# Kernel optimization log

Measured on AMD Instinct MI355X. Metric: run time of the kernel, lower is better.

Reference implementation:

```python
import jax, jax.numpy as jnp
import numpy as np

B, L, D, H, U = 1024, 256, 256, 512, 512


def setup_inputs() -> dict:
    key = jax.random.key(0)
    ks = jax.random.split(key, 5)
    scale_f = 1.0
    return {
        "features": jax.random.normal(ks[0], (B, L, D), dtype=jnp.float32),
        "hidden": jax.random.normal(ks[1], (B, H), dtype=jnp.float32),
        "W1": jax.random.normal(ks[2], (D, U), dtype=jnp.float32) / np.sqrt(D),
        "b1": jnp.zeros((U,), dtype=jnp.float32),
        "W2": jax.random.normal(ks[3], (H, U), dtype=jnp.float32) / np.sqrt(H),
        "b2": jnp.zeros((U,), dtype=jnp.float32),
        "Wv": jax.random.normal(ks[4], (U, 1), dtype=jnp.float32) / np.sqrt(U),
        "bv": jnp.zeros((1,), dtype=jnp.float32),
    }


def reference(features, hidden, W1, b1, W2, b2, Wv, bv):
    # features: [B, L, D], hidden: [B, H]
    proj_f = jnp.einsum("bld,du->blu", features, W1) + b1      # [B, L, U]
    proj_h = (hidden @ W2 + b2)[:, None, :]                      # [B, 1, U]
    score = jnp.tanh(proj_f + proj_h)                            # [B, L, U]
    logits = jnp.einsum("blu,uo->blo", score, Wv) + bv           # [B, L, 1]
    attention_weights = jax.nn.softmax(logits, axis=1)           # [B, L, 1]
    context_vector = jnp.sum(attention_weights * features, axis=1)  # [B, D]
    return (context_vector, attention_weights)
```

## Files before the change

### kernel.cpp

```cpp
#include <hip/hip_runtime.h>
#include <hip/hip_bf16.h>

#define B_ 1024
#define L_ 256
#define D_ 256
#define H_ 512
#define U_ 512
#define M_ (B_ * L_)

#define BM 128

typedef float f32x4 __attribute__((ext_vector_type(4)));
typedef short bf16x8 __attribute__((ext_vector_type(8)));
typedef short bf16x4 __attribute__((ext_vector_type(4)));

__device__ __forceinline__ short f2bf(float f) {
  unsigned u = __float_as_uint(f);
  u += 0x7fffu + ((u >> 16) & 1u);
  return (short)(u >> 16);
}

__device__ __forceinline__ float fast_tanh(float x) {
  float e = __expf(2.0f * x);
  return 1.0f - 2.0f * __builtin_amdgcn_rcpf(e + 1.0f);
}

__global__ void k_w1f(const float* __restrict__ W1, short* __restrict__ W1F) {
  int i = blockIdx.x * 256 + threadIdx.x;
  int jj = i & 7;
  int no = (i >> 3) & 15;
  int kc = (i >> 7) & 3;
  int kb = (i >> 9) & 7;
  int nb = i >> 12;
  int u = nb * 16 + no;
  int d = kb * 32 + kc * 8 + jj;
  W1F[i] = f2bf(W1[(size_t)d * U_ + u]);
}

__global__ void k_projh(const float* __restrict__ hidden, const float* __restrict__ W2,
                        const float* __restrict__ b1, const float* __restrict__ b2,
                        float* __restrict__ ph) {
  int u = blockIdx.x * 256 + threadIdx.x;
  int b0 = blockIdx.y * 8;
  float acc[8] = {0.f, 0.f, 0.f, 0.f, 0.f, 0.f, 0.f, 0.f};
  for (int h = 0; h < H_; ++h) {
    float w = W2[(size_t)h * U_ + u];
#pragma unroll
    for (int i = 0; i < 8; ++i) acc[i] = fmaf(hidden[(size_t)(b0 + i) * H_ + h], w, acc[i]);
  }
  float bias = b1[u] + b2[u];
#pragma unroll
  for (int i = 0; i < 8; ++i) ph[(size_t)(b0 + i) * U_ + u] = acc[i] + bias;
}

__global__ __launch_bounds__(256, 2) void k_gemm(
    const float* __restrict__ F,
    const short* __restrict__ W1F,
    const float* __restrict__ ph,
    const float* __restrict__ Wv,
    float* __restrict__ logits) {
  __shared__ __align__(16) short As[BM * D_];
  __shared__ float csum[2][BM];

  const int tid = threadIdx.x;
  const int lane = tid & 63;
  const int hi = lane >> 4;
  const int wid = tid >> 6;
  const int wr = wid >> 1, wc = wid & 1;
  const int m0 = blockIdx.x * BM;
  const int b = m0 >> 8;

  {
    const float* sp = F + (size_t)(m0 + (tid >> 6)) * D_ + (tid & 63) * 4;
    const int kq8 = (tid & 63) * 8;
#pragma unroll
    for (int jb = 0; jb < 2; ++jb) {
      f32x4 sv[16];
#pragma unroll
      for (int j = 0; j < 16; ++j)
        sv[j] = *(const f32x4*)(sp + (size_t)(jb * 16 + j) * 4 * D_);
#pragma unroll
      for (int j = 0; j < 16; ++j) {
        int row = (jb * 16 + j) * 4 + (tid >> 6);
        int boff = (row * 512 + kq8) ^ ((row & 7) << 4);
        bf16x4 w;
#pragma unroll
        for (int q = 0; q < 4; ++q) w[q] = f2bf(sv[j][q]);
        *(bf16x4*)((char*)As + boff) = w;
      }
    }
  }
  __syncthreads();

  f32x4 acc[4][4];
  float cs[4][4];
  const f32x4 fz = {0.f, 0.f, 0.f, 0.f};
#pragma unroll
  for (int mi = 0; mi < 4; ++mi)
#pragma unroll
    for (int x = 0; x < 4; ++x) { acc[mi][x] = fz; cs[mi][x] = 0.f; }

  const short* bbase = W1F + (size_t)(wc * 32) * 512 + lane * 8;
  bf16x8 bcur[4], bnxt[4];
#pragma unroll
  for (int ni = 0; ni < 4; ++ni)
    bcur[ni] = *(const bf16x8*)(bbase + (size_t)(ni * 8) * 512);

  const float* phr = ph + (size_t)b * U_;
  const int rbase = wr * 64 + (lane & 15);

  for (int nt = 0; nt < 4; ++nt) {
#pragma unroll
    for (int kt = 0; kt < 8; ++kt) {
      if (nt * 8 + kt < 31) {
        const int ktn = (kt + 1) & 7;
        const int ntn64 = (nt + ((kt + 1) >> 3)) * 64;
#pragma unroll
        for (int ni = 0; ni < 4; ++ni)
          bnxt[ni] = *(const bf16x8*)(bbase + (size_t)(ntn64 + ni * 8 + ktn) * 512);
      }
      bf16x8 af[4];
#pragma unroll
      for (int mi = 0; mi < 4; ++mi) {
        int rA = rbase + mi * 16;
        int boff = (rA * 512 + kt * 64 + hi * 16) ^ ((rA & 7) << 4);
        af[mi] = *(const bf16x8*)((const char*)As + boff);
      }
#pragma unroll
      for (int mi = 0; mi < 4; ++mi) {
        acc[mi][0] = __builtin_amdgcn_mfma_f32_16x16x32_bf16(af[mi], bcur[0], acc[mi][0], 0, 0, 0);
        acc[mi][1] = __builtin_amdgcn_mfma_f32_16x16x32_bf16(af[mi], bcur[1], acc[mi][1], 0, 0, 0);
        acc[mi][2] = __builtin_amdgcn_mfma_f32_16x16x32_bf16(af[mi], bcur[2], acc[mi][2], 0, 0, 0);
        acc[mi][3] = __builtin_amdgcn_mfma_f32_16x16x32_bf16(af[mi], bcur[3], acc[mi][3], 0, 0, 0);
      }
#pragma unroll
      for (int ni = 0; ni < 4; ++ni) bcur[ni] = bnxt[ni];
    }
#pragma unroll
    for (int ni = 0; ni < 4; ++ni) {
      int u = nt * 128 + wc * 64 + ni * 16 + (lane & 15);
      float phv = phr[u];
      float wvv = Wv[u];
#pragma unroll
      for (int mi = 0; mi < 4; ++mi) {
#pragma unroll
        for (int r = 0; r < 4; ++r) {
          float x = acc[mi][ni][r] + phv;
          cs[mi][r] += fast_tanh(x) * wvv;
        }
      }
    }
#pragma unroll
    for (int mi = 0; mi < 4; ++mi)
#pragma unroll
      for (int x = 0; x < 4; ++x) acc[mi][x] = fz;
  }

#pragma unroll
  for (int mi = 0; mi < 4; ++mi) {
#pragma unroll
    for (int off = 1; off < 16; off <<= 1) {
#pragma unroll
      for (int r = 0; r < 4; ++r) cs[mi][r] += __shfl_xor(cs[mi][r], off);
    }
    if ((lane & 15) == 0) {
      int rloc = wr * 64 + mi * 16 + hi * 4;
#pragma unroll
      for (int r = 0; r < 4; ++r) csum[wc][rloc + r] = cs[mi][r];
    }
  }
  __syncthreads();
  if (tid < BM) logits[m0 + tid] = csum[0][tid] + csum[1][tid];
}

__global__ void k_smctx(const float* __restrict__ logits, const float* __restrict__ F,
                        float* __restrict__ outw, float* __restrict__ ctx) {
  __shared__ float wl[L_];
  __shared__ f32x4 part[256];
  __shared__ float red[8];
  int b = blockIdx.x, t = threadIdx.x;
  float x = logits[(size_t)b * L_ + t];
  float m = x;
#pragma unroll
  for (int off = 32; off >= 1; off >>= 1) m = fmaxf(m, __shfl_xor(m, off));
  if ((t & 63) == 0) red[t >> 6] = m;
  __syncthreads();
  m = fmaxf(fmaxf(red[0], red[1]), fmaxf(red[2], red[3]));
  float e = __expf(x - m);
  float s = e;
#pragma unroll
  for (int off = 32; off >= 1; off >>= 1) s += __shfl_xor(s, off);
  if ((t & 63) == 0) red[4 + (t >> 6)] = s;
  __syncthreads();
  s = (red[4] + red[5]) + (red[6] + red[7]);
  float w = e / s;
  outw[(size_t)b * L_ + t] = w;
  wl[t] = w;
  __syncthreads();

  int lq = t >> 6, dq = t & 63;
  const f32x4* F4 = (const f32x4*)(F + (size_t)b * L_ * D_);
  f32x4 acc = {0.f, 0.f, 0.f, 0.f};
  for (int l = lq; l < L_; l += 4) acc += wl[l] * F4[l * 64 + dq];
  part[t] = acc;
  __syncthreads();
  if (lq == 0) {
    f32x4 r = (part[t] + part[t + 64]) + (part[t + 128] + part[t + 192]);
    ((f32x4*)ctx)[(size_t)b * 64 + dq] = r;
  }
}

extern "C" void kernel_launch(void* const* d_in, const int* in_sizes, int n_in,
                              void* d_out, int out_size, void* d_ws, size_t ws_size,
                              hipStream_t stream) {
  const float* F      = (const float*)d_in[0];
  const float* hidden = (const float*)d_in[1];
  const float* W1     = (const float*)d_in[2];
  const float* b1     = (const float*)d_in[3];
  const float* W2     = (const float*)d_in[4];
  const float* b2     = (const float*)d_in[5];
  const float* Wv     = (const float*)d_in[6];

  float* out_ctx = (float*)d_out;
  float* out_w   = out_ctx + (size_t)B_ * D_;

  char* ws = (char*)d_ws;
  short* W1F    = (short*)ws;
  float* ph     = (float*)(ws + 262144);
  float* logits = (float*)(ws + 262144 + 2097152);

  k_w1f<<<512, 256, 0, stream>>>(W1, W1F);
  k_projh<<<dim3(2, 128), 256, 0, stream>>>(hidden, W2, b1, b2, ph);
  k_gemm<<<2048, 256, 0, stream>>>(F, W1F, ph, Wv, logits);
  k_smctx<<<1024, 256, 0, stream>>>(logits, F, out_w, out_ctx);
}
```

Before: 254.8 us.

## Split GEMM over N tiles with direct global A loads and atomic logit accumulation

```diff
diff --git a/kernel.cpp b/kernel.cpp
--- a/kernel.cpp
+++ b/kernel.cpp
@@ -12,7 +12,6 @@
 
 typedef float f32x4 __attribute__((ext_vector_type(4)));
 typedef short bf16x8 __attribute__((ext_vector_type(8)));
-typedef short bf16x4 __attribute__((ext_vector_type(4)));
 
 __device__ __forceinline__ short f2bf(float f) {
   unsigned u = __float_as_uint(f);
@@ -53,13 +52,12 @@
   for (int i = 0; i < 8; ++i) ph[(size_t)(b0 + i) * U_ + u] = acc[i] + bias;
 }
 
-__global__ __launch_bounds__(256, 2) void k_gemm(
+__global__ __launch_bounds__(256, 3) void k_gemm(
     const float* __restrict__ F,
     const short* __restrict__ W1F,
     const float* __restrict__ ph,
     const float* __restrict__ Wv,
     float* __restrict__ logits) {
-  __shared__ __align__(16) short As[BM * D_];
   __shared__ float csum[2][BM];
 
   const int tid = threadIdx.x;
@@ -67,95 +65,71 @@
   const int hi = lane >> 4;
   const int wid = tid >> 6;
   const int wr = wid >> 1, wc = wid & 1;
-  const int m0 = blockIdx.x * BM;
+  const int tile = ((blockIdx.x & 7) << 10) | (blockIdx.x >> 3);
+  const int ntile = tile & 3;
+  const int mtile = tile >> 2;
+  const int m0 = mtile * BM;
+  const int n0 = ntile * 128;
   const int b = m0 >> 8;
 
-  {
-    const float* sp = F + (size_t)(m0 + (tid >> 6)) * D_ + (tid & 63) * 4;
-    const int kq8 = (tid & 63) * 8;
-#pragma unroll
-    for (int jb = 0; jb < 2; ++jb) {
-      f32x4 sv[16];
-#pragma unroll
-      for (int j = 0; j < 16; ++j)
-        sv[j] = *(const f32x4*)(sp + (size_t)(jb * 16 + j) * 4 * D_);
-#pragma unroll
-      for (int j = 0; j < 16; ++j) {
-        int row = (jb * 16 + j) * 4 + (tid >> 6);
-        int boff = (row * 512 + kq8) ^ ((row & 7) << 4);
-        bf16x4 w;
-#pragma unroll
-        for (int q = 0; q < 4; ++q) w[q] = f2bf(sv[j][q]);
-        *(bf16x4*)((char*)As + boff) = w;
+  const float* ap[4];
+#pragma unroll
+  for (int mi = 0; mi < 4; ++mi)
+    ap[mi] = F + (size_t)(m0 + wr * 64 + mi * 16 + (lane & 15)) * D_ + hi * 8;
+  const short* bp[4];
+#pragma unroll
+  for (int ni = 0; ni < 4; ++ni)
+    bp[ni] = W1F + ((size_t)((n0 >> 4) + wc * 4 + ni) * 8) * 512 + lane * 8;
+
+  f32x4 acc[4][4];
+  const f32x4 fz = {0.f, 0.f, 0.f, 0.f};
+#pragma unroll
+  for (int mi = 0; mi < 4; ++mi)
+#pragma unroll
+    for (int ni = 0; ni < 4; ++ni) acc[mi][ni] = fz;
+
+#pragma unroll
+  for (int kt = 0; kt < 8; ++kt) {
+    bf16x8 af[4], bfr[4];
+#pragma unroll
+    for (int mi = 0; mi < 4; ++mi) {
+      f32x4 lo = *(const f32x4*)(ap[mi] + kt * 32);
+      f32x4 hi4 = *(const f32x4*)(ap[mi] + kt * 32 + 4);
+      bf16x8 a;
+#pragma unroll
+      for (int j = 0; j < 4; ++j) { a[j] = f2bf(lo[j]); a[4 + j] = f2bf(hi4[j]); }
+      af[mi] = a;
+    }
+#pragma unroll
+    for (int ni = 0; ni < 4; ++ni)
+      bfr[ni] = *(const bf16x8*)(bp[ni] + (size_t)kt * 512);
+#pragma unroll
+    for (int mi = 0; mi < 4; ++mi)
+#pragma unroll
+      for (int ni = 0; ni < 4; ++ni)
+        acc[mi][ni] = __builtin_amdgcn_mfma_f32_16x16x32_bf16(af[mi], bfr[ni], acc[mi][ni], 0, 0, 0);
+  }
+
+  const float* phr = ph + (size_t)b * U_;
+  float cs[4][4];
+#pragma unroll
+  for (int mi = 0; mi < 4; ++mi)
+#pragma unroll
+    for (int r = 0; r < 4; ++r) cs[mi][r] = 0.f;
+#pragma unroll
+  for (int ni = 0; ni < 4; ++ni) {
+    int u = n0 + wc * 64 + ni * 16 + (lane & 15);
+    float phv = phr[u];
+    float wvv = Wv[u];
+#pragma unroll
+    for (int mi = 0; mi < 4; ++mi) {
+#pragma unroll
+      for (int r = 0; r < 4; ++r) {
+        float x = acc[mi][ni][r] + phv;
+        cs[mi][r] += fast_tanh(x) * wvv;
       }
     }
   }
-  __syncthreads();
-
-  f32x4 acc[4][4];
-  float cs[4][4];
-  const f32x4 fz = {0.f, 0.f, 0.f, 0.f};
-#pragma unroll
-  for (int mi = 0; mi < 4; ++mi)
-#pragma unroll
-    for (int x = 0; x < 4; ++x) { acc[mi][x] = fz; cs[mi][x] = 0.f; }
-
-  const short* bbase = W1F + (size_t)(wc * 32) * 512 + lane * 8;
-  bf16x8 bcur[4], bnxt[4];
-#pragma unroll
-  for (int ni = 0; ni < 4; ++ni)
-    bcur[ni] = *(const bf16x8*)(bbase + (size_t)(ni * 8) * 512);
-
-  const float* phr = ph + (size_t)b * U_;
-  const int rbase = wr * 64 + (lane & 15);
-
-  for (int nt = 0; nt < 4; ++nt) {
-#pragma unroll
-    for (int kt = 0; kt < 8; ++kt) {
-      if (nt * 8 + kt < 31) {
-        const int ktn = (kt + 1) & 7;
-        const int ntn64 = (nt + ((kt + 1) >> 3)) * 64;
-#pragma unroll
-        for (int ni = 0; ni < 4; ++ni)
-          bnxt[ni] = *(const bf16x8*)(bbase + (size_t)(ntn64 + ni * 8 + ktn) * 512);
-      }
-      bf16x8 af[4];
-#pragma unroll
-      for (int mi = 0; mi < 4; ++mi) {
-        int rA = rbase + mi * 16;
-        int boff = (rA * 512 + kt * 64 + hi * 16) ^ ((rA & 7) << 4);
-        af[mi] = *(const bf16x8*)((const char*)As + boff);
-      }
-#pragma unroll
-      for (int mi = 0; mi < 4; ++mi) {
-        acc[mi][0] = __builtin_amdgcn_mfma_f32_16x16x32_bf16(af[mi], bcur[0], acc[mi][0], 0, 0, 0);
-        acc[mi][1] = __builtin_amdgcn_mfma_f32_16x16x32_bf16(af[mi], bcur[1], acc[mi][1], 0, 0, 0);
-        acc[mi][2] = __builtin_amdgcn_mfma_f32_16x16x32_bf16(af[mi], bcur[2], acc[mi][2], 0, 0, 0);
-        acc[mi][3] = __builtin_amdgcn_mfma_f32_16x16x32_bf16(af[mi], bcur[3], acc[mi][3], 0, 0, 0);
-      }
-#pragma unroll
-      for (int ni = 0; ni < 4; ++ni) bcur[ni] = bnxt[ni];
-    }
-#pragma unroll
-    for (int ni = 0; ni < 4; ++ni) {
-      int u = nt * 128 + wc * 64 + ni * 16 + (lane & 15);
-      float phv = phr[u];
-      float wvv = Wv[u];
-#pragma unroll
-      for (int mi = 0; mi < 4; ++mi) {
-#pragma unroll
-        for (int r = 0; r < 4; ++r) {
-          float x = acc[mi][ni][r] + phv;
-          cs[mi][r] += fast_tanh(x) * wvv;
-        }
-      }
-    }
-#pragma unroll
-    for (int mi = 0; mi < 4; ++mi)
-#pragma unroll
-      for (int x = 0; x < 4; ++x) acc[mi][x] = fz;
-  }
-
 #pragma unroll
   for (int mi = 0; mi < 4; ++mi) {
 #pragma unroll
@@ -170,7 +144,7 @@
     }
   }
   __syncthreads();
-  if (tid < BM) logits[m0 + tid] = csum[0][tid] + csum[1][tid];
+  if (tid < BM) atomicAdd(&logits[m0 + tid], csum[0][tid] + csum[1][tid]);
 }
 
 __global__ void k_smctx(const float* __restrict__ logits, const float* __restrict__ F,
@@ -229,8 +203,9 @@
   float* ph     = (float*)(ws + 262144);
   float* logits = (float*)(ws + 262144 + 2097152);
 
+  hipMemsetAsync(logits, 0, (size_t)M_ * sizeof(float), stream);
   k_w1f<<<512, 256, 0, stream>>>(W1, W1F);
   k_projh<<<dim3(2, 128), 256, 0, stream>>>(hidden, W2, b1, b2, ph);
-  k_gemm<<<2048, 256, 0, stream>>>(F, W1F, ph, Wv, logits);
+  k_gemm<<<8192, 256, 0, stream>>>(F, W1F, ph, Wv, logits);
   k_smctx<<<1024, 256, 0, stream>>>(logits, F, out_w, out_ctx);
 }
```

New measurement: 395.8 us. 1.55x slower.
